# Kernel tuning notes

Measured on AMD Instinct MI355X. Metric: run time of the kernel, lower is better.

The kernel has to match this reference:

```python
import math
import jax, jax.numpy as jnp
import numpy as np

N_HEADS = 16
D_MODEL = 1024
B, S = 1, 2048


def setup_inputs() -> dict:
    key = jax.random.key(0)
    ks = jax.random.split(key, 8)
    stdv = 1.0 / math.sqrt(D_MODEL)
    def w(k):
        return jax.random.uniform(k, (D_MODEL, D_MODEL), jnp.float32, -stdv, stdv)
    return {
        "query": jax.random.normal(ks[0], (B, S, D_MODEL), jnp.float32),
        "key": jax.random.normal(ks[1], (B, S, D_MODEL), jnp.float32),
        "value": jax.random.normal(ks[2], (B, S, D_MODEL), jnp.float32),
        "attn_mask": jax.random.randint(ks[3], (B, S, S), 0, 2, jnp.int32),
        "W_q": w(ks[4]),
        "W_k": w(ks[5]),
        "W_v": w(ks[6]),
        "W_o": w(ks[7]),
    }


def reference(query, key, value, attn_mask, W_q, W_k, W_v, W_o):
    b = query.shape[0]
    d = D_MODEL // N_HEADS
    # F.linear(x, W) = x @ W.T
    def proj(x, W):
        y = jnp.einsum('bse,de->bsd', x, W)  # [B,S,D]
        return y.reshape(b, -1, N_HEADS, d).transpose(0, 2, 1, 3)  # [B,H,S,d]
    q = proj(query, W_q)
    k = proj(key, W_k)
    v = proj(value, W_v)
    scores = jnp.einsum('bhsd,bhtd->bhst', q, k) / math.sqrt(d)  # [B,H,S,S]
    # masked_fill with -1e-07 where mask is truthy (faithful to source)
    mask = (attn_mask != 0)[:, None, :, :]  # broadcast over heads
    scores = jnp.where(mask, jnp.float32(-1e-07), scores)
    attn_scores = jax.nn.softmax(scores, axis=-1)
    # Faithful quirk: output uses PRE-softmax scores, not attn_scores
    out = jnp.einsum('bhst,bhtd->bhsd', scores, v)
    concat = out.transpose(0, 2, 1, 3).reshape(b, -1, D_MODEL)
    output = jnp.einsum('bse,de->bsd', concat, W_o)
    return output, attn_scores
```

## Files before the change

### kernel.cpp

```cpp
#include <hip/hip_runtime.h>

#define S 2048
#define DM 1024
#define H 16
#define DH 64

typedef __attribute__((ext_vector_type(8))) short bf16x8;
typedef __attribute__((ext_vector_type(4))) float f32x4;
typedef __attribute__((ext_vector_type(4))) unsigned short u16x4;
typedef unsigned short u16;
typedef unsigned int u32;

__device__ __forceinline__ void split2(float x, u16& h, u16& l) {
  const u32 u = __float_as_uint(x);
  const u32 hu = u & 0xFFFF0000u;
  h = (u16)(hu >> 16);
  const float rem = x - __uint_as_float(hu);
  u32 r = __float_as_uint(rem);
  r += 0x7FFFu + ((r >> 16) & 1u);
  l = (u16)(r >> 16);
}

__device__ __forceinline__ void split2v(float x, u16x4& h4, u16x4& l4, int i) {
  u16 hh, ll;
  split2(x, hh, ll);
  h4[i] = hh; l4[i] = ll;
}

__device__ __forceinline__ f32x4 mfma3(bf16x8 ah, bf16x8 al, bf16x8 bh, bf16x8 bl, f32x4 c) {
  c = __builtin_amdgcn_mfma_f32_16x16x32_bf16(ah, bh, c, 0, 0, 0);
  c = __builtin_amdgcn_mfma_f32_16x16x32_bf16(ah, bl, c, 0, 0, 0);
  c = __builtin_amdgcn_mfma_f32_16x16x32_bf16(al, bh, c, 0, 0, 0);
  return c;
}

__global__ __launch_bounds__(256)
void qkv_proj(const float* __restrict__ q, const float* __restrict__ k,
              const float* __restrict__ v, const float* __restrict__ Wq,
              const float* __restrict__ Wk, const float* __restrict__ Wv,
              u16* __restrict__ qh, u16* __restrict__ ql,
              u16* __restrict__ kh, u16* __restrict__ kl,
              u16* __restrict__ vTh, u16* __restrict__ vTl)
{
  __shared__ u16 Ah[128][40], Al[128][40], Bh[128][40], Bl[128][40];
  const int tid = threadIdx.x;
  const int lane = tid & 63, w = tid >> 6;
  const int wr = w >> 1, wc = w & 1;
  const int lg = lane >> 4, lt = lane & 15;
  const int z = blockIdx.z;

  const float *A, *B;
  int m0, n0;
  if (z == 2) { A = Wv; B = v; m0 = blockIdx.y * 128; n0 = blockIdx.x * 128; }
  else {
    A = (z == 0) ? q : k; B = (z == 0) ? Wq : Wk;
    m0 = blockIdx.x * 128; n0 = blockIdx.y * 128;
  }

  f32x4 acc[4][4] = {};

  for (int k0 = 0; k0 < DM; k0 += 32) {
    float4 av[4], bv[4];
#pragma unroll
    for (int p = 0; p < 4; p++) {
      const int idx = p * 256 + tid;
      const int row = idx >> 3, c4 = (idx & 7) * 4;
      av[p] = *(const float4*)&A[(size_t)(m0 + row) * DM + k0 + c4];
      bv[p] = *(const float4*)&B[(size_t)(n0 + row) * DM + k0 + c4];
    }
    __syncthreads();
#pragma unroll
    for (int p = 0; p < 4; p++) {
      const int idx = p * 256 + tid;
      const int row = idx >> 3, c4 = (idx & 7) * 4;
      u16x4 h4, l4;
      split2v(av[p].x, h4, l4, 0); split2v(av[p].y, h4, l4, 1);
      split2v(av[p].z, h4, l4, 2); split2v(av[p].w, h4, l4, 3);
      *(u16x4*)&Ah[row][c4] = h4; *(u16x4*)&Al[row][c4] = l4;
      split2v(bv[p].x, h4, l4, 0); split2v(bv[p].y, h4, l4, 1);
      split2v(bv[p].z, h4, l4, 2); split2v(bv[p].w, h4, l4, 3);
      *(u16x4*)&Bh[row][c4] = h4; *(u16x4*)&Bl[row][c4] = l4;
    }
    __syncthreads();

    bf16x8 bhf[4], blf[4];
#pragma unroll
    for (int fj = 0; fj < 4; fj++) {
      const int r = wc * 64 + fj * 16 + lt;
      bhf[fj] = *(const bf16x8*)&Bh[r][lg * 8];
      blf[fj] = *(const bf16x8*)&Bl[r][lg * 8];
    }
#pragma unroll
    for (int fi = 0; fi < 4; fi++) {
      const int r = wr * 64 + fi * 16 + lt;
      const bf16x8 ahf = *(const bf16x8*)&Ah[r][lg * 8];
      const bf16x8 alf = *(const bf16x8*)&Al[r][lg * 8];
#pragma unroll
      for (int fj = 0; fj < 4; fj++)
        acc[fi][fj] = mfma3(ahf, alf, bhf[fj], blf[fj], acc[fi][fj]);
    }
  }

  u16 *dh, *dl;
  float scale;
  if (z == 0)      { dh = qh;  dl = ql;  scale = 0.125f; }
  else if (z == 1) { dh = kh;  dl = kl;  scale = 1.0f; }
  else             { dh = vTh; dl = vTl; scale = 1.0f; }

#pragma unroll
  for (int fi = 0; fi < 4; fi++)
#pragma unroll
    for (int r = 0; r < 4; r++) {
      const int m = m0 + wr * 64 + fi * 16 + lg * 4 + r;
#pragma unroll
      for (int fj = 0; fj < 4; fj++) {
        const int n = n0 + wc * 64 + fj * 16 + lt;
        const size_t addr = (z == 2) ? ((size_t)m * S + n)
                                     : ((size_t)((n >> 6) * S + m) * 64 + (n & 63));
        u16 hh, ll;
        split2(acc[fi][fj][r] * scale, hh, ll);
        dh[addr] = hh; dl[addr] = ll;
      }
    }
}

__global__ __launch_bounds__(256)
void attn_pv(const u16* __restrict__ qh, const u16* __restrict__ ql,
             const u16* __restrict__ kh, const u16* __restrict__ kl,
             const u16* __restrict__ vTh, const u16* __restrict__ vTl,
             const int* __restrict__ mask,
             float* __restrict__ attn, u16* __restrict__ ch, u16* __restrict__ cl)
{
  __shared__ u16 Kh[64][72], Kl[64][72];
  __shared__ u16 Vh[64][72], Vl[64][72];
  __shared__ u16 Ph[64][72], Pl[64][72];
  const int tid = threadIdx.x;
  const int lane = tid & 63, w = tid >> 6;
  const int lg = lane >> 4, lt = lane & 15;
  const int h = blockIdx.y, s0 = blockIdx.x * 64;
  const int qrow = s0 + w * 16 + lt;

  const size_t qbase = ((size_t)h * S + qrow) * 64;
  bf16x8 Qh_[2], Ql_[2];
  Qh_[0] = *(const bf16x8*)&qh[qbase + lg * 8];
  Qh_[1] = *(const bf16x8*)&qh[qbase + 32 + lg * 8];
  Ql_[0] = *(const bf16x8*)&ql[qbase + lg * 8];
  Ql_[1] = *(const bf16x8*)&ql[qbase + 32 + lg * 8];

  const size_t kbase = (size_t)h * S * 64;
  const size_t vbase = (size_t)h * 64 * S;

  f32x4 ao[4] = {};

  for (int t0 = 0; t0 < S; t0 += 64) {
    __syncthreads();
#pragma unroll
    for (int p = 0; p < 2; p++) {
      const int chunk = p * 256 + tid;
      const int row = chunk >> 3, c8 = (chunk & 7) * 8;
      *(uint4*)&Kh[row][c8] = *(const uint4*)&kh[kbase + (size_t)(t0 + row) * 64 + c8];
      *(uint4*)&Kl[row][c8] = *(const uint4*)&kl[kbase + (size_t)(t0 + row) * 64 + c8];
      *(uint4*)&Vh[row][c8] = *(const uint4*)&vTh[vbase + (size_t)row * S + t0 + c8];
      *(uint4*)&Vl[row][c8] = *(const uint4*)&vTl[vbase + (size_t)row * S + t0 + c8];
    }
    __syncthreads();

    f32x4 sct[4] = {};
#pragma unroll
    for (int ks = 0; ks < 2; ks++) {
#pragma unroll
      for (int ft = 0; ft < 4; ft++) {
        const bf16x8 ah = *(const bf16x8*)&Kh[ft * 16 + lt][ks * 32 + lg * 8];
        const bf16x8 al = *(const bf16x8*)&Kl[ft * 16 + lt][ks * 32 + lg * 8];
        sct[ft] = mfma3(ah, al, Qh_[ks], Ql_[ks], sct[ft]);
      }
    }

    const int* mrow = &mask[(size_t)qrow * S + t0];
    float* arow = &attn[((size_t)h * S + qrow) * S + t0];
#pragma unroll
    for (int ft = 0; ft < 4; ft++) {
      const int tl = ft * 16 + lg * 4;
      const int4 mv = *(const int4*)&mrow[tl];
      f32x4 sv = sct[ft];
      sv[0] = mv.x ? -1e-7f : sv[0];
      sv[1] = mv.y ? -1e-7f : sv[1];
      sv[2] = mv.z ? -1e-7f : sv[2];
      sv[3] = mv.w ? -1e-7f : sv[3];
      *(float4*)&arow[tl] = make_float4(sv[0], sv[1], sv[2], sv[3]);
      u16x4 h4, l4;
      split2v(sv[0], h4, l4, 0); split2v(sv[1], h4, l4, 1);
      split2v(sv[2], h4, l4, 2); split2v(sv[3], h4, l4, 3);
      *(u16x4*)&Ph[w * 16 + lt][tl] = h4;
      *(u16x4*)&Pl[w * 16 + lt][tl] = l4;
    }

#pragma unroll
    for (int ks = 0; ks < 2; ks++) {
      const bf16x8 pa_h = *(const bf16x8*)&Ph[w * 16 + lt][ks * 32 + lg * 8];
      const bf16x8 pa_l = *(const bf16x8*)&Pl[w * 16 + lt][ks * 32 + lg * 8];
#pragma unroll
      for (int fd = 0; fd < 4; fd++) {
        const bf16x8 vb_h = *(const bf16x8*)&Vh[fd * 16 + lt][ks * 32 + lg * 8];
        const bf16x8 vb_l = *(const bf16x8*)&Vl[fd * 16 + lt][ks * 32 + lg * 8];
        ao[fd] = mfma3(pa_h, pa_l, vb_h, vb_l, ao[fd]);
      }
    }
  }

#pragma unroll
  for (int fd = 0; fd < 4; fd++)
#pragma unroll
    for (int r = 0; r < 4; r++) {
      const int qg = s0 + w * 16 + lg * 4 + r;
      const int d = h * 64 + fd * 16 + lt;
      u16 hh, ll;
      split2(ao[fd][r], hh, ll);
      ch[(size_t)qg * DM + d] = hh;
      cl[(size_t)qg * DM + d] = ll;
    }
}

__global__ __launch_bounds__(256)
void softmax_fix(float* __restrict__ attn)
{
  float* row = attn + (size_t)blockIdx.x * S;
  const int tid = threadIdx.x;
  float4 a = ((const float4*)row)[tid];
  float4 b = ((const float4*)row)[tid + 256];

  float m = fmaxf(fmaxf(fmaxf(a.x, a.y), fmaxf(a.z, a.w)),
                  fmaxf(fmaxf(b.x, b.y), fmaxf(b.z, b.w)));
#pragma unroll
  for (int off = 32; off >= 1; off >>= 1)
    m = fmaxf(m, __shfl_xor(m, off));
  __shared__ float redm[4], reds[4];
  if ((tid & 63) == 0) redm[tid >> 6] = m;
  __syncthreads();
  m = fmaxf(fmaxf(redm[0], redm[1]), fmaxf(redm[2], redm[3]));

  a.x = __expf(a.x - m); a.y = __expf(a.y - m);
  a.z = __expf(a.z - m); a.w = __expf(a.w - m);
  b.x = __expf(b.x - m); b.y = __expf(b.y - m);
  b.z = __expf(b.z - m); b.w = __expf(b.w - m);
  float s = a.x + a.y + a.z + a.w + b.x + b.y + b.z + b.w;
#pragma unroll
  for (int off = 32; off >= 1; off >>= 1)
    s += __shfl_xor(s, off);
  if ((tid & 63) == 0) reds[tid >> 6] = s;
  __syncthreads();
  s = reds[0] + reds[1] + reds[2] + reds[3];

  const float inv = 1.0f / s;
  a.x *= inv; a.y *= inv; a.z *= inv; a.w *= inv;
  b.x *= inv; b.y *= inv; b.z *= inv; b.w *= inv;
  ((float4*)row)[tid] = a;
  ((float4*)row)[tid + 256] = b;
}

__global__ __launch_bounds__(256)
void out_proj(const u16* __restrict__ ch, const u16* __restrict__ cl,
              const float* __restrict__ Wo, float* __restrict__ out)
{
  __shared__ u16 Ah[128][40], Al[128][40], Bh[128][40], Bl[128][40];
  const int tid = threadIdx.x;
  const int lane = tid & 63, w = tid >> 6;
  const int wr = w >> 1, wc = w & 1;
  const int lg = lane >> 4, lt = lane & 15;
  const int m0 = blockIdx.x * 128, n0 = blockIdx.y * 128;

  f32x4 acc[4][4] = {};

  for (int k0 = 0; k0 < DM; k0 += 32) {
    uint4 ahv[2], alv[2];
    float4 bv[4];
#pragma unroll
    for (int p = 0; p < 2; p++) {
      const int chunk = p * 256 + tid;
      const int row = chunk >> 2, c8 = (chunk & 3) * 8;
      ahv[p] = *(const uint4*)&ch[(size_t)(m0 + row) * DM + k0 + c8];
      alv[p] = *(const uint4*)&cl[(size_t)(m0 + row) * DM + k0 + c8];
    }
#pragma unroll
    for (int p = 0; p < 4; p++) {
      const int idx = p * 256 + tid;
      const int row = idx >> 3, c4 = (idx & 7) * 4;
      bv[p] = *(const float4*)&Wo[(size_t)(n0 + row) * DM + k0 + c4];
    }
    __syncthreads();
#pragma unroll
    for (int p = 0; p < 2; p++) {
      const int chunk = p * 256 + tid;
      const int row = chunk >> 2, c8 = (chunk & 3) * 8;
      *(uint4*)&Ah[row][c8] = ahv[p];
      *(uint4*)&Al[row][c8] = alv[p];
    }
#pragma unroll
    for (int p = 0; p < 4; p++) {
      const int idx = p * 256 + tid;
      const int row = idx >> 3, c4 = (idx & 7) * 4;
      u16x4 h4, l4;
      split2v(bv[p].x, h4, l4, 0); split2v(bv[p].y, h4, l4, 1);
      split2v(bv[p].z, h4, l4, 2); split2v(bv[p].w, h4, l4, 3);
      *(u16x4*)&Bh[row][c4] = h4; *(u16x4*)&Bl[row][c4] = l4;
    }
    __syncthreads();

    bf16x8 bhf[4], blf[4];
#pragma unroll
    for (int fj = 0; fj < 4; fj++) {
      const int r = wc * 64 + fj * 16 + lt;
      bhf[fj] = *(const bf16x8*)&Bh[r][lg * 8];
      blf[fj] = *(const bf16x8*)&Bl[r][lg * 8];
    }
#pragma unroll
    for (int fi = 0; fi < 4; fi++) {
      const int r = wr * 64 + fi * 16 + lt;
      const bf16x8 ahf = *(const bf16x8*)&Ah[r][lg * 8];
      const bf16x8 alf = *(const bf16x8*)&Al[r][lg * 8];
#pragma unroll
      for (int fj = 0; fj < 4; fj++)
        acc[fi][fj] = mfma3(ahf, alf, bhf[fj], blf[fj], acc[fi][fj]);
    }
  }

#pragma unroll
  for (int fi = 0; fi < 4; fi++)
#pragma unroll
    for (int r = 0; r < 4; r++) {
      const int m = m0 + wr * 64 + fi * 16 + lg * 4 + r;
#pragma unroll
      for (int fj = 0; fj < 4; fj++) {
        const int n = n0 + wc * 64 + fj * 16 + lt;
        out[(size_t)m * DM + n] = acc[fi][fj][r];
      }
    }
}

extern "C" void kernel_launch(void* const* d_in, const int* in_sizes, int n_in,
                              void* d_out, int out_size, void* d_ws, size_t ws_size,
                              hipStream_t stream)
{
  const float* query = (const float*)d_in[0];
  const float* key   = (const float*)d_in[1];
  const float* value = (const float*)d_in[2];
  const int*   mask  = (const int*)d_in[3];
  const float* Wq    = (const float*)d_in[4];
  const float* Wk    = (const float*)d_in[5];
  const float* Wv    = (const float*)d_in[6];
  const float* Wo    = (const float*)d_in[7];

  float* out  = (float*)d_out;
  float* attn = out + (size_t)S * DM;

  const size_t NE = (size_t)H * S * 64;
  u16* qh  = (u16*)d_ws;
  u16* ql  = qh  + NE;
  u16* kh  = ql  + NE;
  u16* kl  = kh  + NE;
  u16* vTh = kl  + NE;
  u16* vTl = vTh + NE;
  u16* ch  = vTl + NE;
  u16* cl  = ch  + NE;

  hipLaunchKernelGGL(qkv_proj, dim3(16, 8, 3), dim3(256), 0, stream,
                     query, key, value, Wq, Wk, Wv, qh, ql, kh, kl, vTh, vTl);

  hipLaunchKernelGGL(attn_pv, dim3(S / 64, H), dim3(256), 0, stream,
                     qh, ql, kh, kl, vTh, vTl, mask, attn, ch, cl);

  hipLaunchKernelGGL(softmax_fix, dim3(H * S), dim3(256), 0, stream, attn);

  hipLaunchKernelGGL(out_proj, dim3(16, 8), dim3(256), 0, stream,
                     ch, cl, Wo, out);
}
```

Measured before the change: 615.0 us.

## Fuse softmax into attention kernel via online max/sum and recompute pass

```diff
diff --git a/kernel.cpp b/kernel.cpp
--- a/kernel.cpp
+++ b/kernel.cpp
@@ -151,6 +151,7 @@
   const size_t vbase = (size_t)h * 64 * S;
 
   f32x4 ao[4] = {};
+  float m_run = -3.0e38f, l_run = 0.0f;
 
   for (int t0 = 0; t0 < S; t0 += 64) {
     __syncthreads();
@@ -177,7 +178,7 @@
     }
 
     const int* mrow = &mask[(size_t)qrow * S + t0];
-    float* arow = &attn[((size_t)h * S + qrow) * S + t0];
+    float pm = -3.0e38f;
 #pragma unroll
     for (int ft = 0; ft < 4; ft++) {
       const int tl = ft * 16 + lg * 4;
@@ -187,13 +188,28 @@
       sv[1] = mv.y ? -1e-7f : sv[1];
       sv[2] = mv.z ? -1e-7f : sv[2];
       sv[3] = mv.w ? -1e-7f : sv[3];
-      *(float4*)&arow[tl] = make_float4(sv[0], sv[1], sv[2], sv[3]);
+      sct[ft] = sv;
+      pm = fmaxf(pm, fmaxf(fmaxf(sv[0], sv[1]), fmaxf(sv[2], sv[3])));
       u16x4 h4, l4;
       split2v(sv[0], h4, l4, 0); split2v(sv[1], h4, l4, 1);
       split2v(sv[2], h4, l4, 2); split2v(sv[3], h4, l4, 3);
       *(u16x4*)&Ph[w * 16 + lt][tl] = h4;
       *(u16x4*)&Pl[w * 16 + lt][tl] = l4;
     }
+
+    pm = fmaxf(pm, __shfl_xor(pm, 16));
+    pm = fmaxf(pm, __shfl_xor(pm, 32));
+    const float mn = fmaxf(m_run, pm);
+    float es = 0.0f;
+#pragma unroll
+    for (int ft = 0; ft < 4; ft++) {
+      es += __expf(sct[ft][0] - mn) + __expf(sct[ft][1] - mn)
+          + __expf(sct[ft][2] - mn) + __expf(sct[ft][3] - mn);
+    }
+    es += __shfl_xor(es, 16);
+    es += __shfl_xor(es, 32);
+    l_run = l_run * __expf(m_run - mn) + es;
+    m_run = mn;
 
 #pragma unroll
     for (int ks = 0; ks < 2; ks++) {
@@ -219,43 +235,50 @@
       ch[(size_t)qg * DM + d] = hh;
       cl[(size_t)qg * DM + d] = ll;
     }
-}
-
-__global__ __launch_bounds__(256)
-void softmax_fix(float* __restrict__ attn)
-{
-  float* row = attn + (size_t)blockIdx.x * S;
-  const int tid = threadIdx.x;
-  float4 a = ((const float4*)row)[tid];
-  float4 b = ((const float4*)row)[tid + 256];
-
-  float m = fmaxf(fmaxf(fmaxf(a.x, a.y), fmaxf(a.z, a.w)),
-                  fmaxf(fmaxf(b.x, b.y), fmaxf(b.z, b.w)));
-#pragma unroll
-  for (int off = 32; off >= 1; off >>= 1)
-    m = fmaxf(m, __shfl_xor(m, off));
-  __shared__ float redm[4], reds[4];
-  if ((tid & 63) == 0) redm[tid >> 6] = m;
-  __syncthreads();
-  m = fmaxf(fmaxf(redm[0], redm[1]), fmaxf(redm[2], redm[3]));
-
-  a.x = __expf(a.x - m); a.y = __expf(a.y - m);
-  a.z = __expf(a.z - m); a.w = __expf(a.w - m);
-  b.x = __expf(b.x - m); b.y = __expf(b.y - m);
-  b.z = __expf(b.z - m); b.w = __expf(b.w - m);
-  float s = a.x + a.y + a.z + a.w + b.x + b.y + b.z + b.w;
-#pragma unroll
-  for (int off = 32; off >= 1; off >>= 1)
-    s += __shfl_xor(s, off);
-  if ((tid & 63) == 0) reds[tid >> 6] = s;
-  __syncthreads();
-  s = reds[0] + reds[1] + reds[2] + reds[3];
-
-  const float inv = 1.0f / s;
-  a.x *= inv; a.y *= inv; a.z *= inv; a.w *= inv;
-  b.x *= inv; b.y *= inv; b.z *= inv; b.w *= inv;
-  ((float4*)row)[tid] = a;
-  ((float4*)row)[tid + 256] = b;
+
+  const float fm  = m_run;
+  const float fil = 1.0f / l_run;
+
+  for (int t0 = 0; t0 < S; t0 += 64) {
+    __syncthreads();
+#pragma unroll
+    for (int p = 0; p < 2; p++) {
+      const int chunk = p * 256 + tid;
+      const int row = chunk >> 3, c8 = (chunk & 7) * 8;
+      *(uint4*)&Kh[row][c8] = *(const uint4*)&kh[kbase + (size_t)(t0 + row) * 64 + c8];
+      *(uint4*)&Kl[row][c8] = *(const uint4*)&kl[kbase + (size_t)(t0 + row) * 64 + c8];
+    }
+    __syncthreads();
+
+    f32x4 sct[4] = {};
+#pragma unroll
+    for (int ks = 0; ks < 2; ks++) {
+#pragma unroll
+      for (int ft = 0; ft < 4; ft++) {
+        const bf16x8 ah = *(const bf16x8*)&Kh[ft * 16 + lt][ks * 32 + lg * 8];
+        const bf16x8 al = *(const bf16x8*)&Kl[ft * 16 + lt][ks * 32 + lg * 8];
+        sct[ft] = mfma3(ah, al, Qh_[ks], Ql_[ks], sct[ft]);
+      }
+    }
+
+    const int* mrow = &mask[(size_t)qrow * S + t0];
+    float* arow = &attn[((size_t)h * S + qrow) * S + t0];
+#pragma unroll
+    for (int ft = 0; ft < 4; ft++) {
+      const int tl = ft * 16 + lg * 4;
+      const int4 mv = *(const int4*)&mrow[tl];
+      f32x4 sv = sct[ft];
+      sv[0] = mv.x ? -1e-7f : sv[0];
+      sv[1] = mv.y ? -1e-7f : sv[1];
+      sv[2] = mv.z ? -1e-7f : sv[2];
+      sv[3] = mv.w ? -1e-7f : sv[3];
+      const float4 o = make_float4(__expf(sv[0] - fm) * fil,
+                                   __expf(sv[1] - fm) * fil,
+                                   __expf(sv[2] - fm) * fil,
+                                   __expf(sv[3] - fm) * fil);
+      *(float4*)&arow[tl] = o;
+    }
+  }
 }
 
 __global__ __launch_bounds__(256)
@@ -369,8 +392,6 @@
   hipLaunchKernelGGL(attn_pv, dim3(S / 64, H), dim3(256), 0, stream,
                      qh, ql, kh, kl, vTh, vTl, mask, attn, ch, cl);
 
-  hipLaunchKernelGGL(softmax_fix, dim3(H * S), dim3(256), 0, stream, attn);
-
   hipLaunchKernelGGL(out_proj, dim3(16, 8), dim3(256), 0, stream,
                      ch, cl, Wo, out);
 }
```

Result: faster. 579.6 us (-5.8%).
